# Performance work log

Measured on AMD Instinct MI355X. Metric: run time of the kernel, lower is better.

Reference implementation:

```python
import jax, jax.numpy as jnp
import numpy as np

M1 = M2 = M3 = 8  # truncated Hartley modes (min(modes, in_channels) in original)


def dht(x):
    # Discrete Hartley transform via 3D FFT over spatial axes: real - imag
    r = jnp.fft.fftn(x, axes=(2, 3, 4))
    return r.real - r.imag


def _mul(a, w):
    # 'bixyz,ioxyz->boxyz' mode-wise channel mixing
    return jnp.einsum('bixyz,ioxyz->boxyz', a, w)


def setup_inputs() -> dict:
    key = jax.random.key(0)
    ks = jax.random.split(key, 5)
    B, Ci, Co = 2, 64, 64
    S1 = S2 = S3 = 64
    scale = 1.0 / (Ci * Co)
    x = jax.random.normal(ks[0], (B, Ci, S1, S2, S3), dtype=jnp.float32)
    wshape = (Ci, Co, M1, M2, M3)
    w1 = scale * jax.random.uniform(ks[1], wshape, dtype=jnp.float32)
    w2 = scale * jax.random.uniform(ks[2], wshape, dtype=jnp.float32)
    w3 = scale * jax.random.uniform(ks[3], wshape, dtype=jnp.float32)
    w4 = scale * jax.random.uniform(ks[4], wshape, dtype=jnp.float32)
    return {"x": x, "w1": w1, "w2": w2, "w3": w3, "w4": w4}


def reference(x, w1, w2, w3, w4):
    b, ci, s1, s2, s3 = x.shape
    co = w1.shape[1]
    # Hartley transform of x ("cos part") and of fully flipped x ("sin part")
    xh = dht(x)
    xhf = dht(x[:, :, ::-1, ::-1, ::-1])

    out_ht = jnp.zeros((b, co, s1, s2, s3), dtype=x.dtype)
    out_ht = out_ht.at[:, :, :M1, :M2, :M3].set(_mul(xh[:, :, :M1, :M2, :M3], w1))
    out_ht = out_ht.at[:, :, -M1:, :M2, :M3].set(_mul(xh[:, :, -M1:, :M2, :M3], w2))
    out_ht = out_ht.at[:, :, :M1, -M2:, :M3].set(_mul(xh[:, :, :M1, -M2:, :M3], w3))
    out_ht = out_ht.at[:, :, -M1:, -M2:, :M3].set(_mul(xh[:, :, -M1:, -M2:, :M3], w4))
    # original zeroes out_ht[:, :, M1:, M2:, M3:] — already zero here since 2*modes <= size

    # inverse DHT = DHT / (D*M*N)
    x_rec = dht(out_ht) / (s1 * s2 * s3)

    # phase = angle(complex(cos_part, sin_part)) = atan2(sin, cos), only on corner block; 0 elsewhere
    phase_corner = jnp.arctan2(xhf[:, :, :M1, :M2, :M3], xh[:, :, :M1, :M2, :M3])
    cos_phase = jnp.ones((b, ci, s1, s2, s3), dtype=x.dtype)
    cos_phase = cos_phase.at[:, :, :M1, :M2, :M3].set(jnp.cos(phase_corner))
    return x_rec * cos_phase
```

## Files before the change

kernel.cpp:

```cpp
#include <hip/hip_runtime.h>
#include <math.h>

struct cf2 { float x, y; };
struct TW64 { float c[64], s[64]; };
struct CF2T { cf2 v[64]; };

constexpr double PI_D = 3.14159265358979323846264338327950288;

constexpr double tsin(double x){
  double x2 = x*x, r = x, t = x;
  t *= -x2/6.0;   r += t;
  t *= -x2/20.0;  r += t;
  t *= -x2/42.0;  r += t;
  t *= -x2/72.0;  r += t;
  t *= -x2/110.0; r += t;
  t *= -x2/156.0; r += t;
  t *= -x2/210.0; r += t;
  t *= -x2/272.0; r += t;
  return r;
}
constexpr double tcos(double x){
  double x2 = x*x, r = 1.0, t = 1.0;
  t *= -x2/2.0;   r += t;
  t *= -x2/12.0;  r += t;
  t *= -x2/30.0;  r += t;
  t *= -x2/56.0;  r += t;
  t *= -x2/90.0;  r += t;
  t *= -x2/132.0; r += t;
  t *= -x2/182.0; r += t;
  t *= -x2/240.0; r += t;
  return r;
}
constexpr double ang_cos(int j){
  int r = j & 15, q = (j >> 4) & 3;
  double a = PI_D/32.0 * r;
  double cc = tcos(a), ss = tsin(a);
  return q==0 ? cc : q==1 ? -ss : q==2 ? -cc : ss;
}
constexpr double ang_sin(int j){
  int r = j & 15, q = (j >> 4) & 3;
  double a = PI_D/32.0 * r;
  double cc = tcos(a), ss = tsin(a);
  return q==0 ? ss : q==1 ? cc : q==2 ? -ss : -cc;
}
constexpr TW64 make_tw(){
  TW64 t{};
  for (int j=0;j<64;j++){ t.c[j] = (float)ang_cos(j); t.s[j] = (float)ang_sin(j); }
  return t;
}
constexpr CF2T make_twi(){
  CF2T r{};
  for (int j=0;j<64;j++){ r.v[j].x = (float)ang_cos(j); r.v[j].y = (float)ang_sin(j); }
  return r;
}
constexpr CF2T make_pq(){
  CF2T r{};
  for (int j=0;j<64;j++){
    double c = ang_cos(j), s = ang_sin(j);
    r.v[j].x = (float)((c + s) / 262144.0);
    r.v[j].y = (float)((s - c) / 262144.0);
  }
  return r;
}

constexpr TW64 TWct = make_tw();
__constant__ CF2T TWIdev = make_twi();
__constant__ CF2T PQdev  = make_pq();


template<int G>
__device__ __forceinline__ void stageA4(const float* __restrict__ row, int sw, float* a){
  #pragma unroll
  for (int m=0;m<8;m++) a[m]=0.f;
  #pragma unroll
  for (int qd=0;qd<16;qd++){
    float4 v = ((const float4*)row)[qd ^ sw];
    float xv[4] = {v.x, v.y, v.z, v.w};
    #pragma unroll
    for (int u=0;u<4;u++){
      int n3 = qd*4 + u;
      #pragma unroll
      for (int m=0;m<4;m++){
        a[2*m  ] = fmaf(xv[u],  TWct.c[((G+m)*n3)&63], a[2*m  ]);
        a[2*m+1] = fmaf(xv[u], -TWct.s[((G+m)*n3)&63], a[2*m+1]);
      }
    }
  }
}

__global__ __launch_bounds__(256) void k_fwd(const float* __restrict__ x, float2* __restrict__ y2g){
  __shared__ alignas(16) float xt[2][64][64];
  __shared__ alignas(16) float2 y1[2][8][66];
  __shared__ cf2 twl[64];
  int bid = blockIdx.x;
  int pp = bid & 31, ci_b = bid >> 5;
  int t = threadIdx.x;
  if (t < 64) twl[t] = TWIdev.v[t];

  const float4* src = (const float4*)(x + (size_t)(ci_b*64 + pp*2)*4096);
  #pragma unroll
  for (int j=0;j<8;j++){
    int q = t + j*256;
    float4 v = src[q];
    int n1l = q >> 10, r = q & 1023;
    int n2 = r >> 4, n3q = r & 15;
    float* d = &xt[n1l][n2][(n3q ^ (n2 & 7))*4];
    d[0]=v.x; d[1]=v.y; d[2]=v.z; d[3]=v.w;
  }
  __syncthreads();

  {
    int n2 = t & 63, g = (t>>6)&1, n1l = t>>7;
    const float* row = &xt[n1l][n2][0];
    int sw = n2 & 7;
    float a[8];
    if (g==0) stageA4<0>(row, sw, a); else stageA4<4>(row, sw, a);
    #pragma unroll
    for (int m=0;m<4;m++) y1[n1l][4*g+m][n2] = make_float2(a[2*m], a[2*m+1]);
  }
  __syncthreads();

  {
    int n1l = t>>7, s = t&127, k2i = s>>3, k3 = s&7;
    int k2 = k2i<8 ? k2i : 48+k2i;
    cf2 st = twl[k2];
    float c = 1.f, sn = 0.f, ar = 0.f, ai = 0.f;
    const float4* yrow = (const float4*)&y1[n1l][k3][0];
    #pragma unroll
    for (int m=0;m<32;m++){
      float4 v = yrow[m];
      ar = fmaf(v.x, c, fmaf(v.y, sn, ar));
      ai = fmaf(v.y, c, fmaf(-v.x, sn, ai));
      float c2 = fmaf(c, st.x, -(sn*st.y));
      float s2 = fmaf(sn, st.x,  c*st.y);
      ar = fmaf(v.z, c2, fmaf(v.w, s2, ar));
      ai = fmaf(v.w, c2, fmaf(-v.z, s2, ai));
      c  = fmaf(c2, st.x, -(s2*st.y));
      sn = fmaf(s2, st.x,  c2*st.y);
    }
    y2g[(size_t)(ci_b*64 + pp*2 + n1l)*128 + s] = make_float2(ar, ai);
  }
}

__global__ __launch_bounds__(256) void k_fwd_n1(const float2* __restrict__ y2g,
                                                float* __restrict__ xh, float* __restrict__ cp){
  __shared__ alignas(16) float2 yl[64][8];
  __shared__ cf2 twl[64];
  int bc = blockIdx.x >> 4, k2i = blockIdx.x & 15;
  int t = threadIdx.x;
  if (t < 64) twl[t] = TWIdev.v[t];
  {
    int n1 = t >> 2, q = t & 3;
    const float4* s4 = (const float4*)(y2g + ((size_t)(bc*64 + n1)*128 + k2i*8));
    ((float4*)&yl[n1][0])[q] = s4[q];
  }
  __syncthreads();
  int half = t&1, k3 = (t>>1)&7, k1i = t>>4;
  int k1 = k1i<8 ? k1i : 48+k1i;
  cf2 st = twl[k1];
  cf2 cs = twl[(k1*half*32)&63];
  float c = cs.x, sn = cs.y, ar = 0.f, ai = 0.f;
  #pragma unroll
  for (int i=0;i<32;i++){
    float2 y = yl[half*32+i][k3];
    ar = fmaf(y.x, c, fmaf(y.y, sn, ar));
    ai = fmaf(y.y, c, fmaf(-y.x, sn, ai));
    float c2 = fmaf(c, st.x, -(sn*st.y));
    sn = fmaf(sn, st.x,  c*st.y);
    c = c2;
  }
  ar += __shfl_xor(ar, 1, 64);
  ai += __shfl_xor(ai, 1, 64);
  if (half == 0){
    float vxh = ar - ai;
    xh[(size_t)(bc*16 + k1i)*128 + k2i*8 + k3] = vxh;
    if (k1i < 8 && k2i < 8){
      cf2 tw = twl[(k1i + k2i + k3) & 63];
      float vxhf = ar*(tw.x - tw.y) + ai*(tw.x + tw.y);
      cp[(size_t)bc*512 + k1i*64 + k2i*8 + k3] = cosf(atan2f(vxhf, vxh));
    }
  }
}

__global__ __launch_bounds__(256) void k_mix(const float* __restrict__ xh,
    const float* __restrict__ w1, const float* __restrict__ w2,
    const float* __restrict__ w3, const float* __restrict__ w4,
    float* __restrict__ mh){
  __shared__ alignas(16) float xs[2][64][64];
  __shared__ alignas(16) float wsh[64][64];
  __shared__ float ps[2][128];
  int bid = blockIdx.x;
  int k1l = bid & 7, co = (bid >> 3) & 63, blk = bid >> 9;
  const float* w = (blk==0) ? w1 : (blk==1) ? w2 : (blk==2) ? w3 : w4;
  int k1i = k1l + ((blk & 1) << 3);
  int k2off = (blk & 2) ? 64 : 0;
  int t = threadIdx.x;
  #pragma unroll
  for (int jj=0;jj<4;jj++){
    int idx = t + jj*256;
    int ci = idx >> 4, kq = idx & 15;
    float4 v = *(const float4*)(w + (size_t)(ci*64 + co)*512 + k1l*64 + kq*4);
    ((float4*)&wsh[ci][0])[kq] = v;
  }
  #pragma unroll
  for (int jj=0;jj<8;jj++){
    int idx = t + jj*256;
    int b = idx >> 10, ci = (idx >> 4) & 63, kq = idx & 15;
    float4 v = *(const float4*)(xh + (size_t)((b*64 + ci)*16 + k1i)*128 + k2off + kq*4);
    ((float4*)&xs[b][ci][0])[kq] = v;
  }
  __syncthreads();
  int half = t >> 7, o = t & 127, b = o >> 6, kk = o & 63;
  float acc = 0.f;
  #pragma unroll 8
  for (int i=0;i<32;i++){
    int ci = half*32 + i;
    acc = fmaf(xs[b][ci][kk], wsh[ci][kk], acc);
  }
  ps[half][o] = acc;
  __syncthreads();
  if (t < 128){
    int b2 = t >> 6, kk2 = t & 63;
    mh[(size_t)((b2*64 + co)*16 + k1i)*128 + k2off + kk2] = ps[0][t] + ps[1][t];
  }
}

__global__ __launch_bounds__(256) void k_inv(const float* __restrict__ mh,
                                             const float* __restrict__ cp,
                                             float* __restrict__ out){
  __shared__ alignas(16) float ml[2048];
  __shared__ alignas(16) float2 z1[16][8];
  __shared__ alignas(16) float2 z2[64][8];
  __shared__ cf2 twl[64];
  __shared__ cf2 pql[64];
  int bid = blockIdx.x;
  int n1 = bid & 63, bc = bid >> 6;
  int t = threadIdx.x;
  if (t < 64){ twl[t] = TWIdev.v[t]; pql[t] = PQdev.v[t]; }
  const float4* src = (const float4*)(mh + (size_t)bc * 2048);
  ((float4*)ml)[t]       = src[t];
  ((float4*)ml)[t + 256] = src[t + 256];
  __syncthreads();
  if (t < 128){
    float zr = 0.f, zi = 0.f;
    #pragma unroll
    for (int k1i=0;k1i<16;k1i++){
      int k1 = k1i < 8 ? k1i : 48 + k1i;
      cf2 tw = TWIdev.v[(k1*n1)&63];
      float m = ml[k1i*128 + t];
      zr = fmaf(m, tw.x, zr);
      zi = fmaf(m, -tw.y, zi);
    }
    z1[t>>3][t&7] = make_float2(zr, zi);
  }
  __syncthreads();
  #pragma unroll
  for (int jo=0;jo<2;jo++){
    int o = t + jo*256;
    int n2 = o >> 3, k3 = o & 7;
    cf2 st = twl[n2];
    float zr = 0.f, zi = 0.f;
    float c = 1.f, sn = 0.f;
    #pragma unroll
    for (int k2i=0;k2i<8;k2i++){
      float2 z = z1[k2i][k3];
      zr = fmaf(z.x, c, fmaf(z.y, sn, zr));
      zi = fmaf(z.y, c, fmaf(-z.x, sn, zi));
      float c2 = fmaf(c, st.x, -(sn*st.y));
      sn = fmaf(sn, st.x, c*st.y);
      c = c2;
    }
    cf2 cs = twl[(56*n2)&63];
    c = cs.x; sn = cs.y;
    #pragma unroll
    for (int k2i=8;k2i<16;k2i++){
      float2 z = z1[k2i][k3];
      zr = fmaf(z.x, c, fmaf(z.y, sn, zr));
      zi = fmaf(z.y, c, fmaf(-z.x, sn, zi));
      float c2 = fmaf(c, st.x, -(sn*st.y));
      sn = fmaf(sn, st.x, c*st.y);
      c = c2;
    }
    z2[n2][k3] = make_float2(zr, zi);
  }
  __syncthreads();
  int n3p = t & 31;
  int wv = t >> 6, g = (t >> 5) & 1;
  int n30 = 2*n3p, n31 = 2*n3p + 1;
  float p0[8], q0[8], p1[8], q1[8];
  #pragma unroll
  for (int k3=0;k3<8;k3++){
    cf2 a = pql[(k3*n30)&63];
    cf2 b = pql[(k3*n31)&63];
    p0[k3] = a.x; q0[k3] = a.y;
    p1[k3] = b.x; q1[k3] = b.y;
  }
  float* orow = out + ((size_t)bc*64 + n1)*4096;
  const float* cprow = cp + (size_t)bc*512 + n1*64;
  bool corner = (n1 < 8) && (n3p < 4);
  #pragma unroll
  for (int j=0;j<8;j++){
    int n2 = wv*16 + 2*j + g;
    const float4* zr4 = (const float4*)&z2[n2][0];
    float4 u0 = zr4[0], u1 = zr4[1], u2 = zr4[2], u3 = zr4[3];
    float v0, v1;
    v0 = fmaf(u0.x, p0[0], u0.y*q0[0]);
    v0 = fmaf(u0.z, p0[1], fmaf(u0.w, q0[1], v0));
    v0 = fmaf(u1.x, p0[2], fmaf(u1.y, q0[2], v0));
    v0 = fmaf(u1.z, p0[3], fmaf(u1.w, q0[3], v0));
    v0 = fmaf(u2.x, p0[4], fmaf(u2.y, q0[4], v0));
    v0 = fmaf(u2.z, p0[5], fmaf(u2.w, q0[5], v0));
    v0 = fmaf(u3.x, p0[6], fmaf(u3.y, q0[6], v0));
    v0 = fmaf(u3.z, p0[7], fmaf(u3.w, q0[7], v0));
    v1 = fmaf(u0.x, p1[0], u0.y*q1[0]);
    v1 = fmaf(u0.z, p1[1], fmaf(u0.w, q1[1], v1));
    v1 = fmaf(u1.x, p1[2], fmaf(u1.y, q1[2], v1));
    v1 = fmaf(u1.z, p1[3], fmaf(u1.w, q1[3], v1));
    v1 = fmaf(u2.x, p1[4], fmaf(u2.y, q1[4], v1));
    v1 = fmaf(u2.z, p1[5], fmaf(u2.w, q1[5], v1));
    v1 = fmaf(u3.x, p1[6], fmaf(u3.y, q1[6], v1));
    v1 = fmaf(u3.z, p1[7], fmaf(u3.w, q1[7], v1));
    if (corner && n2 < 8){
      v0 *= cprow[n2*8 + n30];
      v1 *= cprow[n2*8 + n31];
    }
    ((float2*)orow)[n2*32 + n3p] = make_float2(v0, v1);
  }
}

extern "C" void kernel_launch(void* const* d_in, const int* in_sizes, int n_in,
                              void* d_out, int out_size, void* d_ws, size_t ws_size,
                              hipStream_t stream) {
  (void)in_sizes; (void)n_in; (void)out_size; (void)ws_size;
  const float* x  = (const float*)d_in[0];
  const float* w1 = (const float*)d_in[1];
  const float* w2 = (const float*)d_in[2];
  const float* w3 = (const float*)d_in[3];
  const float* w4 = (const float*)d_in[4];
  float* out = (float*)d_out;
  char* ws = (char*)d_ws;
  float2* y2g = (float2*)ws;
  float*  xh  = (float*)(ws + (8u<<20));
  float*  cp  = (float*)(ws + (9u<<20));
  float*  mh  = (float*)(ws + (9u<<20) + (256u<<10));

  k_fwd   <<<4096, 256, 0, stream>>>(x, y2g);
  k_fwd_n1<<<2048, 256, 0, stream>>>(y2g, xh, cp);
  k_mix   <<<2048, 256, 0, stream>>>(xh, w1, w2, w3, w4, mh);
  k_inv   <<<8192, 256, 0, stream>>>(mh, cp, out);
}
```

Before: 283.9 us.

## Fuse four kernels into one persistent kernel with grid-wide barriers

Replaces the four separate launches (forward 2D DFT, forward n1 DFT, channel mix, inverse transform) with a single persistent kernel of 512 blocks that loops over tiles and separates the phases with atomic-counter grid barriers. Stage buffers are unioned in shared memory, and the first stage prefetches the next input tile into shared memory while the previous one is processed. This removes launch overheads and inter-kernel gaps, but parallelism drops to 512 blocks and the spin barriers depend on every block being co-resident. The input stage now runs one 64x64 slice per iteration with fewer threads active in the second DFT step.

```diff
diff --git a/kernel.cpp b/kernel.cpp
--- a/kernel.cpp
+++ b/kernel.cpp
@@ -67,11 +67,30 @@
 __constant__ CF2T TWIdev = make_twi();
 __constant__ CF2T PQdev  = make_pq();
 
-
-template<int G>
-__device__ __forceinline__ void stageA4(const float* __restrict__ row, int sw, float* a){
-  #pragma unroll
-  for (int m=0;m<8;m++) a[m]=0.f;
+#define NB 512
+
+__device__ __forceinline__ void gridbar(unsigned* bar){
+  __syncthreads();
+  __threadfence();
+  if (threadIdx.x == 0){
+    atomicAdd(bar, 1u);
+    while (__hip_atomic_load(bar, __ATOMIC_ACQUIRE, __HIP_MEMORY_SCOPE_AGENT) < (unsigned)NB)
+      __builtin_amdgcn_s_sleep(2);
+  }
+  __syncthreads();
+  __threadfence();
+}
+
+union SMem {
+  struct { float xt[64][64]; float2 y1[8][66]; } s1;
+  struct { float2 yl[64][8]; } s2;
+  struct { float wsh[64][64]; float xs[64][64]; float ps[4][64]; } s3;
+  struct { float ml[2048]; float2 z1[16][8]; float2 z2[64][8]; } s4;
+};
+
+template<int K>
+__device__ __forceinline__ void stageA2(const float* __restrict__ row, int sw, float* a){
+  a[0]=a[1]=a[2]=a[3]=0.f;
   #pragma unroll
   for (int qd=0;qd<16;qd++){
     float4 v = ((const float4*)row)[qd ^ sw];
@@ -79,252 +98,270 @@
     #pragma unroll
     for (int u=0;u<4;u++){
       int n3 = qd*4 + u;
-      #pragma unroll
-      for (int m=0;m<4;m++){
-        a[2*m  ] = fmaf(xv[u],  TWct.c[((G+m)*n3)&63], a[2*m  ]);
-        a[2*m+1] = fmaf(xv[u], -TWct.s[((G+m)*n3)&63], a[2*m+1]);
-      }
-    }
-  }
-}
-
-__global__ __launch_bounds__(256) void k_fwd(const float* __restrict__ x, float2* __restrict__ y2g){
-  __shared__ alignas(16) float xt[2][64][64];
-  __shared__ alignas(16) float2 y1[2][8][66];
-  __shared__ cf2 twl[64];
-  int bid = blockIdx.x;
-  int pp = bid & 31, ci_b = bid >> 5;
-  int t = threadIdx.x;
-  if (t < 64) twl[t] = TWIdev.v[t];
-
-  const float4* src = (const float4*)(x + (size_t)(ci_b*64 + pp*2)*4096);
+      a[0] = fmaf(xv[u],  TWct.c[((K  )*n3)&63], a[0]);
+      a[1] = fmaf(xv[u], -TWct.s[((K  )*n3)&63], a[1]);
+      a[2] = fmaf(xv[u],  TWct.c[((K+1)*n3)&63], a[2]);
+      a[3] = fmaf(xv[u], -TWct.s[((K+1)*n3)&63], a[3]);
+    }
+  }
+}
+
+__device__ __forceinline__ void s1_load(const float* __restrict__ x, SMem& sm, int tile, int t){
+  const float4* src = (const float4*)(x + (size_t)tile*4096);
   #pragma unroll
-  for (int j=0;j<8;j++){
+  for (int j=0;j<4;j++){
     int q = t + j*256;
     float4 v = src[q];
-    int n1l = q >> 10, r = q & 1023;
-    int n2 = r >> 4, n3q = r & 15;
-    float* d = &xt[n1l][n2][(n3q ^ (n2 & 7))*4];
+    int n2 = q >> 4, n3q = q & 15;
+    float* d = &sm.s1.xt[n2][(n3q ^ (n2 & 7))*4];
     d[0]=v.x; d[1]=v.y; d[2]=v.z; d[3]=v.w;
   }
-  __syncthreads();
-
-  {
-    int n2 = t & 63, g = (t>>6)&1, n1l = t>>7;
-    const float* row = &xt[n1l][n2][0];
-    int sw = n2 & 7;
-    float a[8];
-    if (g==0) stageA4<0>(row, sw, a); else stageA4<4>(row, sw, a);
-    #pragma unroll
-    for (int m=0;m<4;m++) y1[n1l][4*g+m][n2] = make_float2(a[2*m], a[2*m+1]);
-  }
-  __syncthreads();
-
-  {
-    int n1l = t>>7, s = t&127, k2i = s>>3, k3 = s&7;
-    int k2 = k2i<8 ? k2i : 48+k2i;
-    cf2 st = twl[k2];
-    float c = 1.f, sn = 0.f, ar = 0.f, ai = 0.f;
-    const float4* yrow = (const float4*)&y1[n1l][k3][0];
-    #pragma unroll
-    for (int m=0;m<32;m++){
-      float4 v = yrow[m];
-      ar = fmaf(v.x, c, fmaf(v.y, sn, ar));
-      ai = fmaf(v.y, c, fmaf(-v.x, sn, ai));
-      float c2 = fmaf(c, st.x, -(sn*st.y));
-      float s2 = fmaf(sn, st.x,  c*st.y);
-      ar = fmaf(v.z, c2, fmaf(v.w, s2, ar));
-      ai = fmaf(v.w, c2, fmaf(-v.z, s2, ai));
-      c  = fmaf(c2, st.x, -(s2*st.y));
-      sn = fmaf(s2, st.x,  c2*st.y);
-    }
-    y2g[(size_t)(ci_b*64 + pp*2 + n1l)*128 + s] = make_float2(ar, ai);
-  }
-}
-
-__global__ __launch_bounds__(256) void k_fwd_n1(const float2* __restrict__ y2g,
-                                                float* __restrict__ xh, float* __restrict__ cp){
-  __shared__ alignas(16) float2 yl[64][8];
-  __shared__ cf2 twl[64];
-  int bc = blockIdx.x >> 4, k2i = blockIdx.x & 15;
-  int t = threadIdx.x;
-  if (t < 64) twl[t] = TWIdev.v[t];
-  {
-    int n1 = t >> 2, q = t & 3;
-    const float4* s4 = (const float4*)(y2g + ((size_t)(bc*64 + n1)*128 + k2i*8));
-    ((float4*)&yl[n1][0])[q] = s4[q];
-  }
-  __syncthreads();
-  int half = t&1, k3 = (t>>1)&7, k1i = t>>4;
-  int k1 = k1i<8 ? k1i : 48+k1i;
-  cf2 st = twl[k1];
-  cf2 cs = twl[(k1*half*32)&63];
-  float c = cs.x, sn = cs.y, ar = 0.f, ai = 0.f;
-  #pragma unroll
-  for (int i=0;i<32;i++){
-    float2 y = yl[half*32+i][k3];
-    ar = fmaf(y.x, c, fmaf(y.y, sn, ar));
-    ai = fmaf(y.y, c, fmaf(-y.x, sn, ai));
-    float c2 = fmaf(c, st.x, -(sn*st.y));
-    sn = fmaf(sn, st.x,  c*st.y);
-    c = c2;
-  }
-  ar += __shfl_xor(ar, 1, 64);
-  ai += __shfl_xor(ai, 1, 64);
-  if (half == 0){
-    float vxh = ar - ai;
-    xh[(size_t)(bc*16 + k1i)*128 + k2i*8 + k3] = vxh;
-    if (k1i < 8 && k2i < 8){
-      cf2 tw = twl[(k1i + k2i + k3) & 63];
-      float vxhf = ar*(tw.x - tw.y) + ai*(tw.x + tw.y);
-      cp[(size_t)bc*512 + k1i*64 + k2i*8 + k3] = cosf(atan2f(vxhf, vxh));
-    }
-  }
-}
-
-__global__ __launch_bounds__(256) void k_mix(const float* __restrict__ xh,
+}
+
+__global__ __launch_bounds__(256, 2) void k_all(
+    const float* __restrict__ x,
     const float* __restrict__ w1, const float* __restrict__ w2,
     const float* __restrict__ w3, const float* __restrict__ w4,
-    float* __restrict__ mh){
-  __shared__ alignas(16) float xs[2][64][64];
-  __shared__ alignas(16) float wsh[64][64];
-  __shared__ float ps[2][128];
-  int bid = blockIdx.x;
-  int k1l = bid & 7, co = (bid >> 3) & 63, blk = bid >> 9;
-  const float* w = (blk==0) ? w1 : (blk==1) ? w2 : (blk==2) ? w3 : w4;
-  int k1i = k1l + ((blk & 1) << 3);
-  int k2off = (blk & 2) ? 64 : 0;
-  int t = threadIdx.x;
-  #pragma unroll
-  for (int jj=0;jj<4;jj++){
-    int idx = t + jj*256;
-    int ci = idx >> 4, kq = idx & 15;
-    float4 v = *(const float4*)(w + (size_t)(ci*64 + co)*512 + k1l*64 + kq*4);
-    ((float4*)&wsh[ci][0])[kq] = v;
-  }
-  #pragma unroll
-  for (int jj=0;jj<8;jj++){
-    int idx = t + jj*256;
-    int b = idx >> 10, ci = (idx >> 4) & 63, kq = idx & 15;
-    float4 v = *(const float4*)(xh + (size_t)((b*64 + ci)*16 + k1i)*128 + k2off + kq*4);
-    ((float4*)&xs[b][ci][0])[kq] = v;
-  }
-  __syncthreads();
-  int half = t >> 7, o = t & 127, b = o >> 6, kk = o & 63;
-  float acc = 0.f;
-  #pragma unroll 8
-  for (int i=0;i<32;i++){
-    int ci = half*32 + i;
-    acc = fmaf(xs[b][ci][kk], wsh[ci][kk], acc);
-  }
-  ps[half][o] = acc;
-  __syncthreads();
-  if (t < 128){
-    int b2 = t >> 6, kk2 = t & 63;
-    mh[(size_t)((b2*64 + co)*16 + k1i)*128 + k2off + kk2] = ps[0][t] + ps[1][t];
-  }
-}
-
-__global__ __launch_bounds__(256) void k_inv(const float* __restrict__ mh,
-                                             const float* __restrict__ cp,
-                                             float* __restrict__ out){
-  __shared__ alignas(16) float ml[2048];
-  __shared__ alignas(16) float2 z1[16][8];
-  __shared__ alignas(16) float2 z2[64][8];
+    float2* __restrict__ y2g, float* __restrict__ xh, float* __restrict__ cp,
+    float* __restrict__ mh, float* __restrict__ out, unsigned* __restrict__ bars)
+{
+  __shared__ SMem sm;
   __shared__ cf2 twl[64];
   __shared__ cf2 pql[64];
+  int t = threadIdx.x;
   int bid = blockIdx.x;
-  int n1 = bid & 63, bc = bid >> 6;
-  int t = threadIdx.x;
   if (t < 64){ twl[t] = TWIdev.v[t]; pql[t] = PQdev.v[t]; }
-  const float4* src = (const float4*)(mh + (size_t)bc * 2048);
-  ((float4*)ml)[t]       = src[t];
-  ((float4*)ml)[t + 256] = src[t + 256];
-  __syncthreads();
-  if (t < 128){
-    float zr = 0.f, zi = 0.f;
+
+  {
+    int tile0 = bid * 16;
+    s1_load(x, sm, tile0, t);
+    __syncthreads();
+    #pragma unroll 1
+    for (int i=0;i<16;i++){
+      int tile = tile0 + i;
+      {
+        int n2 = t & 63, g = t >> 6;
+        const float* row = &sm.s1.xt[n2][0];
+        int sw = n2 & 7;
+        float a[4];
+        switch(g){
+          case 0: stageA2<0>(row, sw, a); break;
+          case 1: stageA2<2>(row, sw, a); break;
+          case 2: stageA2<4>(row, sw, a); break;
+          default: stageA2<6>(row, sw, a); break;
+        }
+        sm.s1.y1[2*g  ][n2] = make_float2(a[0], a[1]);
+        sm.s1.y1[2*g+1][n2] = make_float2(a[2], a[3]);
+      }
+      __syncthreads();
+      if (i < 15) s1_load(x, sm, tile+1, t);
+      if (t < 128){
+        int k2i = t>>3, k3 = t&7;
+        int k2 = k2i<8 ? k2i : 48+k2i;
+        cf2 st = twl[k2];
+        float c = 1.f, sn = 0.f, ar = 0.f, ai = 0.f;
+        const float4* yrow = (const float4*)&sm.s1.y1[k3][0];
+        #pragma unroll
+        for (int m=0;m<32;m++){
+          float4 v = yrow[m];
+          ar = fmaf(v.x, c, fmaf(v.y, sn, ar));
+          ai = fmaf(v.y, c, fmaf(-v.x, sn, ai));
+          float c2 = fmaf(c, st.x, -(sn*st.y));
+          float s2 = fmaf(sn, st.x,  c*st.y);
+          ar = fmaf(v.z, c2, fmaf(v.w, s2, ar));
+          ai = fmaf(v.w, c2, fmaf(-v.z, s2, ai));
+          c  = fmaf(c2, st.x, -(s2*st.y));
+          sn = fmaf(s2, st.x,  c2*st.y);
+        }
+        y2g[(size_t)tile*128 + t] = make_float2(ar, ai);
+      }
+      __syncthreads();
+    }
+  }
+  gridbar(bars + 0);
+
+  #pragma unroll 1
+  for (int i=0;i<4;i++){
+    int tile = bid*4 + i;
+    int bc = tile >> 4, k2i = tile & 15;
+    {
+      int n1 = t >> 2, q = t & 3;
+      const float4* s4p = (const float4*)(y2g + ((size_t)(bc*64 + n1)*128 + k2i*8));
+      ((float4*)&sm.s2.yl[n1][0])[q] = s4p[q];
+    }
+    __syncthreads();
+    {
+      int half = t&1, k3 = (t>>1)&7, k1i = t>>4;
+      int k1 = k1i<8 ? k1i : 48+k1i;
+      cf2 st = twl[k1];
+      cf2 cs = twl[(k1*half*32)&63];
+      float c = cs.x, sn = cs.y, ar = 0.f, ai = 0.f;
+      #pragma unroll
+      for (int j=0;j<32;j++){
+        float2 y = sm.s2.yl[half*32+j][k3];
+        ar = fmaf(y.x, c, fmaf(y.y, sn, ar));
+        ai = fmaf(y.y, c, fmaf(-y.x, sn, ai));
+        float c2 = fmaf(c, st.x, -(sn*st.y));
+        sn = fmaf(sn, st.x,  c*st.y);
+        c = c2;
+      }
+      ar += __shfl_xor(ar, 1, 64);
+      ai += __shfl_xor(ai, 1, 64);
+      if (half == 0){
+        float vxh = ar - ai;
+        xh[(size_t)(bc*16 + k1i)*128 + k2i*8 + k3] = vxh;
+        if (k1i < 8 && k2i < 8){
+          cf2 tw = twl[(k1i + k2i + k3) & 63];
+          float vxhf = ar*(tw.x - tw.y) + ai*(tw.x + tw.y);
+          cp[(size_t)bc*512 + k1i*64 + k2i*8 + k3] = cosf(atan2f(vxhf, vxh));
+        }
+      }
+    }
+    __syncthreads();
+  }
+  gridbar(bars + 1);
+
+  #pragma unroll 1
+  for (int i=0;i<4;i++){
+    int tile = bid*4 + i;
+    int k1l = tile & 7, co = (tile >> 3) & 63, blk = tile >> 9;
+    const float* w = (blk==0) ? w1 : (blk==1) ? w2 : (blk==2) ? w3 : w4;
+    int k1i = k1l + ((blk & 1) << 3);
+    int k2off = (blk & 2) ? 64 : 0;
     #pragma unroll
-    for (int k1i=0;k1i<16;k1i++){
-      int k1 = k1i < 8 ? k1i : 48 + k1i;
-      cf2 tw = TWIdev.v[(k1*n1)&63];
-      float m = ml[k1i*128 + t];
-      zr = fmaf(m, tw.x, zr);
-      zi = fmaf(m, -tw.y, zi);
-    }
-    z1[t>>3][t&7] = make_float2(zr, zi);
-  }
-  __syncthreads();
-  #pragma unroll
-  for (int jo=0;jo<2;jo++){
-    int o = t + jo*256;
-    int n2 = o >> 3, k3 = o & 7;
-    cf2 st = twl[n2];
-    float zr = 0.f, zi = 0.f;
-    float c = 1.f, sn = 0.f;
-    #pragma unroll
-    for (int k2i=0;k2i<8;k2i++){
-      float2 z = z1[k2i][k3];
-      zr = fmaf(z.x, c, fmaf(z.y, sn, zr));
-      zi = fmaf(z.y, c, fmaf(-z.x, sn, zi));
-      float c2 = fmaf(c, st.x, -(sn*st.y));
-      sn = fmaf(sn, st.x, c*st.y);
-      c = c2;
-    }
-    cf2 cs = twl[(56*n2)&63];
-    c = cs.x; sn = cs.y;
-    #pragma unroll
-    for (int k2i=8;k2i<16;k2i++){
-      float2 z = z1[k2i][k3];
-      zr = fmaf(z.x, c, fmaf(z.y, sn, zr));
-      zi = fmaf(z.y, c, fmaf(-z.x, sn, zi));
-      float c2 = fmaf(c, st.x, -(sn*st.y));
-      sn = fmaf(sn, st.x, c*st.y);
-      c = c2;
-    }
-    z2[n2][k3] = make_float2(zr, zi);
-  }
-  __syncthreads();
-  int n3p = t & 31;
-  int wv = t >> 6, g = (t >> 5) & 1;
-  int n30 = 2*n3p, n31 = 2*n3p + 1;
-  float p0[8], q0[8], p1[8], q1[8];
-  #pragma unroll
-  for (int k3=0;k3<8;k3++){
-    cf2 a = pql[(k3*n30)&63];
-    cf2 b = pql[(k3*n31)&63];
-    p0[k3] = a.x; q0[k3] = a.y;
-    p1[k3] = b.x; q1[k3] = b.y;
-  }
-  float* orow = out + ((size_t)bc*64 + n1)*4096;
-  const float* cprow = cp + (size_t)bc*512 + n1*64;
-  bool corner = (n1 < 8) && (n3p < 4);
-  #pragma unroll
-  for (int j=0;j<8;j++){
-    int n2 = wv*16 + 2*j + g;
-    const float4* zr4 = (const float4*)&z2[n2][0];
-    float4 u0 = zr4[0], u1 = zr4[1], u2 = zr4[2], u3 = zr4[3];
-    float v0, v1;
-    v0 = fmaf(u0.x, p0[0], u0.y*q0[0]);
-    v0 = fmaf(u0.z, p0[1], fmaf(u0.w, q0[1], v0));
-    v0 = fmaf(u1.x, p0[2], fmaf(u1.y, q0[2], v0));
-    v0 = fmaf(u1.z, p0[3], fmaf(u1.w, q0[3], v0));
-    v0 = fmaf(u2.x, p0[4], fmaf(u2.y, q0[4], v0));
-    v0 = fmaf(u2.z, p0[5], fmaf(u2.w, q0[5], v0));
-    v0 = fmaf(u3.x, p0[6], fmaf(u3.y, q0[6], v0));
-    v0 = fmaf(u3.z, p0[7], fmaf(u3.w, q0[7], v0));
-    v1 = fmaf(u0.x, p1[0], u0.y*q1[0]);
-    v1 = fmaf(u0.z, p1[1], fmaf(u0.w, q1[1], v1));
-    v1 = fmaf(u1.x, p1[2], fmaf(u1.y, q1[2], v1));
-    v1 = fmaf(u1.z, p1[3], fmaf(u1.w, q1[3], v1));
-    v1 = fmaf(u2.x, p1[4], fmaf(u2.y, q1[4], v1));
-    v1 = fmaf(u2.z, p1[5], fmaf(u2.w, q1[5], v1));
-    v1 = fmaf(u3.x, p1[6], fmaf(u3.y, q1[6], v1));
-    v1 = fmaf(u3.z, p1[7], fmaf(u3.w, q1[7], v1));
-    if (corner && n2 < 8){
-      v0 *= cprow[n2*8 + n30];
-      v1 *= cprow[n2*8 + n31];
-    }
-    ((float2*)orow)[n2*32 + n3p] = make_float2(v0, v1);
+    for (int jj=0;jj<4;jj++){
+      int idx = t + jj*256;
+      int ci = idx >> 4, kq = idx & 15;
+      float4 v = *(const float4*)(w + (size_t)(ci*64 + co)*512 + k1l*64 + kq*4);
+      ((float4*)&sm.s3.wsh[ci][0])[kq] = v;
+    }
+    #pragma unroll 1
+    for (int b=0;b<2;b++){
+      #pragma unroll
+      for (int jj=0;jj<4;jj++){
+        int idx = t + jj*256;
+        int ci = idx >> 4, kq = idx & 15;
+        float4 v = *(const float4*)(xh + (size_t)((b*64 + ci)*16 + k1i)*128 + k2off + kq*4);
+        ((float4*)&sm.s3.xs[ci][0])[kq] = v;
+      }
+      __syncthreads();
+      {
+        int quarter = t >> 6, kk = t & 63;
+        float acc = 0.f;
+        #pragma unroll
+        for (int c2=0;c2<16;c2++){
+          int ci = quarter*16 + c2;
+          acc = fmaf(sm.s3.xs[ci][kk], sm.s3.wsh[ci][kk], acc);
+        }
+        sm.s3.ps[quarter][kk] = acc;
+      }
+      __syncthreads();
+      if (t < 64)
+        mh[(size_t)((b*64 + co)*16 + k1i)*128 + k2off + t] =
+          sm.s3.ps[0][t] + sm.s3.ps[1][t] + sm.s3.ps[2][t] + sm.s3.ps[3][t];
+      __syncthreads();
+    }
+  }
+  gridbar(bars + 2);
+
+  {
+    int bc = bid >> 2;
+    const float4* srcm = (const float4*)(mh + (size_t)bc * 2048);
+    ((float4*)sm.s4.ml)[t]       = srcm[t];
+    ((float4*)sm.s4.ml)[t + 256] = srcm[t + 256];
+    __syncthreads();
+    #pragma unroll 1
+    for (int i=0;i<16;i++){
+      int n1 = (bid & 3)*16 + i;
+      if (t < 128){
+        float zr = 0.f, zi = 0.f;
+        #pragma unroll
+        for (int k1i=0;k1i<16;k1i++){
+          int k1 = k1i < 8 ? k1i : 48 + k1i;
+          cf2 tw = TWIdev.v[(k1*n1)&63];
+          float m = sm.s4.ml[k1i*128 + t];
+          zr = fmaf(m, tw.x, zr);
+          zi = fmaf(m, -tw.y, zi);
+        }
+        sm.s4.z1[t>>3][t&7] = make_float2(zr, zi);
+      }
+      __syncthreads();
+      #pragma unroll
+      for (int jo=0;jo<2;jo++){
+        int o = t + jo*256;
+        int n2 = o >> 3, k3 = o & 7;
+        cf2 st = twl[n2];
+        float zr = 0.f, zi = 0.f;
+        float c = 1.f, sn = 0.f;
+        #pragma unroll
+        for (int k2i=0;k2i<8;k2i++){
+          float2 z = sm.s4.z1[k2i][k3];
+          zr = fmaf(z.x, c, fmaf(z.y, sn, zr));
+          zi = fmaf(z.y, c, fmaf(-z.x, sn, zi));
+          float c2 = fmaf(c, st.x, -(sn*st.y));
+          sn = fmaf(sn, st.x, c*st.y);
+          c = c2;
+        }
+        cf2 cs = twl[(56*n2)&63];
+        c = cs.x; sn = cs.y;
+        #pragma unroll
+        for (int k2i=8;k2i<16;k2i++){
+          float2 z = sm.s4.z1[k2i][k3];
+          zr = fmaf(z.x, c, fmaf(z.y, sn, zr));
+          zi = fmaf(z.y, c, fmaf(-z.x, sn, zi));
+          float c2 = fmaf(c, st.x, -(sn*st.y));
+          sn = fmaf(sn, st.x, c*st.y);
+          c = c2;
+        }
+        sm.s4.z2[n2][k3] = make_float2(zr, zi);
+      }
+      __syncthreads();
+      {
+        int n3p = t & 31;
+        int wv = t >> 6, g = (t >> 5) & 1;
+        int n30 = 2*n3p, n31 = 2*n3p + 1;
+        float p0[8], q0[8], p1[8], q1[8];
+        #pragma unroll
+        for (int k3=0;k3<8;k3++){
+          cf2 a = pql[(k3*n30)&63];
+          cf2 b = pql[(k3*n31)&63];
+          p0[k3] = a.x; q0[k3] = a.y;
+          p1[k3] = b.x; q1[k3] = b.y;
+        }
+        float* orow = out + ((size_t)bc*64 + n1)*4096;
+        const float* cprow = cp + (size_t)bc*512 + n1*64;
+        bool corner = (n1 < 8) && (n3p < 4);
+        #pragma unroll
+        for (int j=0;j<8;j++){
+          int n2 = wv*16 + 2*j + g;
+          const float4* zr4 = (const float4*)&sm.s4.z2[n2][0];
+          float4 u0 = zr4[0], u1 = zr4[1], u2 = zr4[2], u3 = zr4[3];
+          float v0, v1;
+          v0 = fmaf(u0.x, p0[0], u0.y*q0[0]);
+          v0 = fmaf(u0.z, p0[1], fmaf(u0.w, q0[1], v0));
+          v0 = fmaf(u1.x, p0[2], fmaf(u1.y, q0[2], v0));
+          v0 = fmaf(u1.z, p0[3], fmaf(u1.w, q0[3], v0));
+          v0 = fmaf(u2.x, p0[4], fmaf(u2.y, q0[4], v0));
+          v0 = fmaf(u2.z, p0[5], fmaf(u2.w, q0[5], v0));
+          v0 = fmaf(u3.x, p0[6], fmaf(u3.y, q0[6], v0));
+          v0 = fmaf(u3.z, p0[7], fmaf(u3.w, q0[7], v0));
+          v1 = fmaf(u0.x, p1[0], u0.y*q1[0]);
+          v1 = fmaf(u0.z, p1[1], fmaf(u0.w, q1[1], v1));
+          v1 = fmaf(u1.x, p1[2], fmaf(u1.y, q1[2], v1));
+          v1 = fmaf(u1.z, p1[3], fmaf(u1.w, q1[3], v1));
+          v1 = fmaf(u2.x, p1[4], fmaf(u2.y, q1[4], v1));
+          v1 = fmaf(u2.z, p1[5], fmaf(u2.w, q1[5], v1));
+          v1 = fmaf(u3.x, p1[6], fmaf(u3.y, q1[6], v1));
+          v1 = fmaf(u3.z, p1[7], fmaf(u3.w, q1[7], v1));
+          if (corner && n2 < 8){
+            v0 *= cprow[n2*8 + n30];
+            v1 *= cprow[n2*8 + n31];
+          }
+          ((float2*)orow)[n2*32 + n3p] = make_float2(v0, v1);
+        }
+      }
+      __syncthreads();
+    }
   }
 }
 
@@ -339,13 +376,13 @@
   const float* w4 = (const float*)d_in[4];
   float* out = (float*)d_out;
   char* ws = (char*)d_ws;
-  float2* y2g = (float2*)ws;
-  float*  xh  = (float*)(ws + (8u<<20));
-  float*  cp  = (float*)(ws + (9u<<20));
-  float*  mh  = (float*)(ws + (9u<<20) + (256u<<10));
-
-  k_fwd   <<<4096, 256, 0, stream>>>(x, y2g);
-  k_fwd_n1<<<2048, 256, 0, stream>>>(y2g, xh, cp);
-  k_mix   <<<2048, 256, 0, stream>>>(xh, w1, w2, w3, w4, mh);
-  k_inv   <<<8192, 256, 0, stream>>>(mh, cp, out);
-}
+  float2*   y2g  = (float2*)ws;
+  float*    xh   = (float*)(ws + (8u<<20));
+  float*    cp   = (float*)(ws + (9u<<20));
+  float*    mh   = (float*)(ws + (9u<<20) + (256u<<10));
+  unsigned* bars = (unsigned*)(ws + (10u<<20) + (512u<<10));
+
+  hipMemsetAsync(bars, 0, 3*sizeof(unsigned), stream);
+
+  k_all<<<NB, 256, 0, stream>>>(x, w1, w2, w3, w4, y2g, xh, cp, mh, out, bars);
+}
```

Result: slower. 631.4 us (+122.4%).

## Split forward DFT stages across more threads and break twiddle recurrence chains

Applied to the files above, without the earlier changes.

k_fwd now handles one (b,ci,n1) plane per block instead of two, launching twice as many blocks. Each thread computes two k3 outputs in stage A instead of four. The k2 stage is split across two half-block groups, combined through shared memory. k_fwd_n1 and k_inv split their serial twiddle-rotation recurrences into two independent chains to expose ILP, and k_mix reads xh directly from global memory across four ci-quarters instead of staging it in shared memory. The aim is more parallelism and shorter dependency chains in these small-DFT stages, at the cost of extra reductions, extra syncs, and less contiguous global reads in k_mix.

```diff
diff --git a/kernel.cpp b/kernel.cpp
--- a/kernel.cpp
+++ b/kernel.cpp
@@ -68,10 +68,9 @@
 __constant__ CF2T PQdev  = make_pq();
 
 
-template<int G>
-__device__ __forceinline__ void stageA4(const float* __restrict__ row, int sw, float* a){
-  #pragma unroll
-  for (int m=0;m<8;m++) a[m]=0.f;
+template<int K>
+__device__ __forceinline__ void stageA2(const float* __restrict__ row, int sw, float* a){
+  a[0]=a[1]=a[2]=a[3]=0.f;
   #pragma unroll
   for (int qd=0;qd<16;qd++){
     float4 v = ((const float4*)row)[qd ^ sw];
@@ -79,66 +78,88 @@
     #pragma unroll
     for (int u=0;u<4;u++){
       int n3 = qd*4 + u;
-      #pragma unroll
-      for (int m=0;m<4;m++){
-        a[2*m  ] = fmaf(xv[u],  TWct.c[((G+m)*n3)&63], a[2*m  ]);
-        a[2*m+1] = fmaf(xv[u], -TWct.s[((G+m)*n3)&63], a[2*m+1]);
-      }
+      a[0] = fmaf(xv[u],  TWct.c[((K  )*n3)&63], a[0]);
+      a[1] = fmaf(xv[u], -TWct.s[((K  )*n3)&63], a[1]);
+      a[2] = fmaf(xv[u],  TWct.c[((K+1)*n3)&63], a[2]);
+      a[3] = fmaf(xv[u], -TWct.s[((K+1)*n3)&63], a[3]);
     }
   }
 }
 
 __global__ __launch_bounds__(256) void k_fwd(const float* __restrict__ x, float2* __restrict__ y2g){
-  __shared__ alignas(16) float xt[2][64][64];
-  __shared__ alignas(16) float2 y1[2][8][66];
+  __shared__ alignas(16) float xt[64][64];
+  __shared__ alignas(16) float2 y1[8][66];
+  __shared__ float2 ps[2][128];
   __shared__ cf2 twl[64];
   int bid = blockIdx.x;
-  int pp = bid & 31, ci_b = bid >> 5;
   int t = threadIdx.x;
   if (t < 64) twl[t] = TWIdev.v[t];
 
-  const float4* src = (const float4*)(x + (size_t)(ci_b*64 + pp*2)*4096);
-  #pragma unroll
-  for (int j=0;j<8;j++){
+  const float4* src = (const float4*)(x + (size_t)bid*4096);
+  #pragma unroll
+  for (int j=0;j<4;j++){
     int q = t + j*256;
     float4 v = src[q];
-    int n1l = q >> 10, r = q & 1023;
-    int n2 = r >> 4, n3q = r & 15;
-    float* d = &xt[n1l][n2][(n3q ^ (n2 & 7))*4];
+    int n2 = q >> 4, n3q = q & 15;
+    float* d = &xt[n2][(n3q ^ (n2 & 7))*4];
     d[0]=v.x; d[1]=v.y; d[2]=v.z; d[3]=v.w;
   }
   __syncthreads();
 
   {
-    int n2 = t & 63, g = (t>>6)&1, n1l = t>>7;
-    const float* row = &xt[n1l][n2][0];
+    int n2 = t & 63, g = t >> 6;
+    const float* row = &xt[n2][0];
     int sw = n2 & 7;
-    float a[8];
-    if (g==0) stageA4<0>(row, sw, a); else stageA4<4>(row, sw, a);
-    #pragma unroll
-    for (int m=0;m<4;m++) y1[n1l][4*g+m][n2] = make_float2(a[2*m], a[2*m+1]);
+    float a[4];
+    switch(g){
+      case 0: stageA2<0>(row, sw, a); break;
+      case 1: stageA2<2>(row, sw, a); break;
+      case 2: stageA2<4>(row, sw, a); break;
+      default: stageA2<6>(row, sw, a); break;
+    }
+    y1[2*g  ][n2] = make_float2(a[0], a[1]);
+    y1[2*g+1][n2] = make_float2(a[2], a[3]);
   }
   __syncthreads();
 
   {
-    int n1l = t>>7, s = t&127, k2i = s>>3, k3 = s&7;
+    int s = t & 127, h = t >> 7;
+    int k2i = s>>3, k3 = s&7;
     int k2 = k2i<8 ? k2i : 48+k2i;
     cf2 st = twl[k2];
-    float c = 1.f, sn = 0.f, ar = 0.f, ai = 0.f;
-    const float4* yrow = (const float4*)&y1[n1l][k3][0];
-    #pragma unroll
-    for (int m=0;m<32;m++){
-      float4 v = yrow[m];
-      ar = fmaf(v.x, c, fmaf(v.y, sn, ar));
-      ai = fmaf(v.y, c, fmaf(-v.x, sn, ai));
-      float c2 = fmaf(c, st.x, -(sn*st.y));
-      float s2 = fmaf(sn, st.x,  c*st.y);
-      ar = fmaf(v.z, c2, fmaf(v.w, s2, ar));
-      ai = fmaf(v.w, c2, fmaf(-v.z, s2, ai));
-      c  = fmaf(c2, st.x, -(s2*st.y));
-      sn = fmaf(s2, st.x,  c2*st.y);
-    }
-    y2g[(size_t)(ci_b*64 + pp*2 + n1l)*128 + s] = make_float2(ar, ai);
+    cf2 i0 = twl[(k2*32*h) & 63];
+    cf2 i1 = twl[(k2*(32*h+16)) & 63];
+    float c0=i0.x, s0=i0.y, ar0=0.f, ai0=0.f;
+    float c1=i1.x, s1=i1.y, ar1=0.f, ai1=0.f;
+    const float4* yrow = (const float4*)&y1[k3][0];
+    #pragma unroll
+    for (int m=0;m<8;m++){
+      float4 v = yrow[16*h + m];
+      ar0 = fmaf(v.x, c0, fmaf(v.y, s0, ar0));
+      ai0 = fmaf(v.y, c0, fmaf(-v.x, s0, ai0));
+      float c0b = fmaf(c0, st.x, -(s0*st.y));
+      float s0b = fmaf(s0, st.x,  c0*st.y);
+      ar0 = fmaf(v.z, c0b, fmaf(v.w, s0b, ar0));
+      ai0 = fmaf(v.w, c0b, fmaf(-v.z, s0b, ai0));
+      c0  = fmaf(c0b, st.x, -(s0b*st.y));
+      s0  = fmaf(s0b, st.x,  c0b*st.y);
+
+      float4 w = yrow[16*h + 8 + m];
+      ar1 = fmaf(w.x, c1, fmaf(w.y, s1, ar1));
+      ai1 = fmaf(w.y, c1, fmaf(-w.x, s1, ai1));
+      float c1b = fmaf(c1, st.x, -(s1*st.y));
+      float s1b = fmaf(s1, st.x,  c1*st.y);
+      ar1 = fmaf(w.z, c1b, fmaf(w.w, s1b, ar1));
+      ai1 = fmaf(w.w, c1b, fmaf(-w.z, s1b, ai1));
+      c1  = fmaf(c1b, st.x, -(s1b*st.y));
+      s1  = fmaf(s1b, st.x,  c1b*st.y);
+    }
+    ps[h][s] = make_float2(ar0+ar1, ai0+ai1);
+  }
+  __syncthreads();
+  if (t < 128){
+    float2 a = ps[0][t], b = ps[1][t];
+    y2g[(size_t)bid*128 + t] = make_float2(a.x+b.x, a.y+b.y);
   }
 }
 
@@ -158,17 +179,26 @@
   int half = t&1, k3 = (t>>1)&7, k1i = t>>4;
   int k1 = k1i<8 ? k1i : 48+k1i;
   cf2 st = twl[k1];
-  cf2 cs = twl[(k1*half*32)&63];
-  float c = cs.x, sn = cs.y, ar = 0.f, ai = 0.f;
-  #pragma unroll
-  for (int i=0;i<32;i++){
-    float2 y = yl[half*32+i][k3];
-    ar = fmaf(y.x, c, fmaf(y.y, sn, ar));
-    ai = fmaf(y.y, c, fmaf(-y.x, sn, ai));
-    float c2 = fmaf(c, st.x, -(sn*st.y));
-    sn = fmaf(sn, st.x,  c*st.y);
-    c = c2;
-  }
+  cf2 i0 = twl[(k1*32*half)&63];
+  cf2 i1 = twl[(k1*(32*half+16))&63];
+  float c0=i0.x, s0=i0.y, ar0=0.f, ai0=0.f;
+  float c1=i1.x, s1=i1.y, ar1=0.f, ai1=0.f;
+  #pragma unroll
+  for (int j=0;j<16;j++){
+    float2 y = yl[half*32+j][k3];
+    ar0 = fmaf(y.x, c0, fmaf(y.y, s0, ar0));
+    ai0 = fmaf(y.y, c0, fmaf(-y.x, s0, ai0));
+    float c0b = fmaf(c0, st.x, -(s0*st.y));
+    s0 = fmaf(s0, st.x,  c0*st.y);
+    c0 = c0b;
+    float2 z = yl[half*32+16+j][k3];
+    ar1 = fmaf(z.x, c1, fmaf(z.y, s1, ar1));
+    ai1 = fmaf(z.y, c1, fmaf(-z.x, s1, ai1));
+    float c1b = fmaf(c1, st.x, -(s1*st.y));
+    s1 = fmaf(s1, st.x,  c1*st.y);
+    c1 = c1b;
+  }
+  float ar = ar0 + ar1, ai = ai0 + ai1;
   ar += __shfl_xor(ar, 1, 64);
   ai += __shfl_xor(ai, 1, 64);
   if (half == 0){
@@ -186,9 +216,8 @@
     const float* __restrict__ w1, const float* __restrict__ w2,
     const float* __restrict__ w3, const float* __restrict__ w4,
     float* __restrict__ mh){
-  __shared__ alignas(16) float xs[2][64][64];
   __shared__ alignas(16) float wsh[64][64];
-  __shared__ float ps[2][128];
+  __shared__ float ps[4][64];
   int bid = blockIdx.x;
   int k1l = bid & 7, co = (bid >> 3) & 63, blk = bid >> 9;
   const float* w = (blk==0) ? w1 : (blk==1) ? w2 : (blk==2) ? w3 : w4;
@@ -202,26 +231,22 @@
     float4 v = *(const float4*)(w + (size_t)(ci*64 + co)*512 + k1l*64 + kq*4);
     ((float4*)&wsh[ci][0])[kq] = v;
   }
-  #pragma unroll
-  for (int jj=0;jj<8;jj++){
-    int idx = t + jj*256;
-    int b = idx >> 10, ci = (idx >> 4) & 63, kq = idx & 15;
-    float4 v = *(const float4*)(xh + (size_t)((b*64 + ci)*16 + k1i)*128 + k2off + kq*4);
-    ((float4*)&xs[b][ci][0])[kq] = v;
-  }
-  __syncthreads();
-  int half = t >> 7, o = t & 127, b = o >> 6, kk = o & 63;
-  float acc = 0.f;
-  #pragma unroll 8
-  for (int i=0;i<32;i++){
-    int ci = half*32 + i;
-    acc = fmaf(xs[b][ci][kk], wsh[ci][kk], acc);
-  }
-  ps[half][o] = acc;
-  __syncthreads();
-  if (t < 128){
-    int b2 = t >> 6, kk2 = t & 63;
-    mh[(size_t)((b2*64 + co)*16 + k1i)*128 + k2off + kk2] = ps[0][t] + ps[1][t];
+  __syncthreads();
+  int quarter = t >> 6, kk = t & 63;
+  #pragma unroll 1
+  for (int b=0;b<2;b++){
+    const float* xb = xh + ((size_t)(b*64 + quarter*16)*16 + k1i)*128 + k2off + kk;
+    float acc = 0.f;
+    #pragma unroll
+    for (int c2=0;c2<16;c2++){
+      acc = fmaf(xb[(size_t)c2*2048], wsh[quarter*16 + c2][kk], acc);
+    }
+    ps[quarter][kk] = acc;
+    __syncthreads();
+    if (t < 64)
+      mh[(size_t)((b*64 + co)*16 + k1i)*128 + k2off + t] =
+        ps[0][t] + ps[1][t] + ps[2][t] + ps[3][t];
+    __syncthreads();
   }
 }
 
@@ -259,72 +284,71 @@
     int o = t + jo*256;
     int n2 = o >> 3, k3 = o & 7;
     cf2 st = twl[n2];
-    float zr = 0.f, zi = 0.f;
-    float c = 1.f, sn = 0.f;
-    #pragma unroll
-    for (int k2i=0;k2i<8;k2i++){
-      float2 z = z1[k2i][k3];
-      zr = fmaf(z.x, c, fmaf(z.y, sn, zr));
-      zi = fmaf(z.y, c, fmaf(-z.x, sn, zi));
-      float c2 = fmaf(c, st.x, -(sn*st.y));
-      sn = fmaf(sn, st.x, c*st.y);
-      c = c2;
-    }
-    cf2 cs = twl[(56*n2)&63];
-    c = cs.x; sn = cs.y;
-    #pragma unroll
-    for (int k2i=8;k2i<16;k2i++){
-      float2 z = z1[k2i][k3];
-      zr = fmaf(z.x, c, fmaf(z.y, sn, zr));
-      zi = fmaf(z.y, c, fmaf(-z.x, sn, zi));
-      float c2 = fmaf(c, st.x, -(sn*st.y));
-      sn = fmaf(sn, st.x, c*st.y);
-      c = c2;
-    }
-    z2[n2][k3] = make_float2(zr, zi);
-  }
-  __syncthreads();
-  int n3p = t & 31;
-  int wv = t >> 6, g = (t >> 5) & 1;
-  int n30 = 2*n3p, n31 = 2*n3p + 1;
-  float p0[8], q0[8], p1[8], q1[8];
-  #pragma unroll
-  for (int k3=0;k3<8;k3++){
-    cf2 a = pql[(k3*n30)&63];
-    cf2 b = pql[(k3*n31)&63];
-    p0[k3] = a.x; q0[k3] = a.y;
-    p1[k3] = b.x; q1[k3] = b.y;
-  }
-  float* orow = out + ((size_t)bc*64 + n1)*4096;
-  const float* cprow = cp + (size_t)bc*512 + n1*64;
-  bool corner = (n1 < 8) && (n3p < 4);
-  #pragma unroll
-  for (int j=0;j<8;j++){
-    int n2 = wv*16 + 2*j + g;
-    const float4* zr4 = (const float4*)&z2[n2][0];
-    float4 u0 = zr4[0], u1 = zr4[1], u2 = zr4[2], u3 = zr4[3];
-    float v0, v1;
-    v0 = fmaf(u0.x, p0[0], u0.y*q0[0]);
-    v0 = fmaf(u0.z, p0[1], fmaf(u0.w, q0[1], v0));
-    v0 = fmaf(u1.x, p0[2], fmaf(u1.y, q0[2], v0));
-    v0 = fmaf(u1.z, p0[3], fmaf(u1.w, q0[3], v0));
-    v0 = fmaf(u2.x, p0[4], fmaf(u2.y, q0[4], v0));
-    v0 = fmaf(u2.z, p0[5], fmaf(u2.w, q0[5], v0));
-    v0 = fmaf(u3.x, p0[6], fmaf(u3.y, q0[6], v0));
-    v0 = fmaf(u3.z, p0[7], fmaf(u3.w, q0[7], v0));
-    v1 = fmaf(u0.x, p1[0], u0.y*q1[0]);
-    v1 = fmaf(u0.z, p1[1], fmaf(u0.w, q1[1], v1));
-    v1 = fmaf(u1.x, p1[2], fmaf(u1.y, q1[2], v1));
-    v1 = fmaf(u1.z, p1[3], fmaf(u1.w, q1[3], v1));
-    v1 = fmaf(u2.x, p1[4], fmaf(u2.y, q1[4], v1));
-    v1 = fmaf(u2.z, p1[5], fmaf(u2.w, q1[5], v1));
-    v1 = fmaf(u3.x, p1[6], fmaf(u3.y, q1[6], v1));
-    v1 = fmaf(u3.z, p1[7], fmaf(u3.w, q1[7], v1));
-    if (corner && n2 < 8){
-      v0 *= cprow[n2*8 + n30];
-      v1 *= cprow[n2*8 + n31];
-    }
-    ((float2*)orow)[n2*32 + n3p] = make_float2(v0, v1);
+    float zr0=0.f, zi0=0.f, zr1=0.f, zi1=0.f;
+    float c0 = 1.f, s0 = 0.f;
+    cf2 i1 = twl[(56*n2)&63];
+    float c1 = i1.x, s1 = i1.y;
+    #pragma unroll
+    for (int k=0;k<8;k++){
+      float2 a = z1[k][k3];
+      zr0 = fmaf(a.x, c0, fmaf(a.y, s0, zr0));
+      zi0 = fmaf(a.y, c0, fmaf(-a.x, s0, zi0));
+      float c0b = fmaf(c0, st.x, -(s0*st.y));
+      s0 = fmaf(s0, st.x, c0*st.y);
+      c0 = c0b;
+      float2 b = z1[8+k][k3];
+      zr1 = fmaf(b.x, c1, fmaf(b.y, s1, zr1));
+      zi1 = fmaf(b.y, c1, fmaf(-b.x, s1, zi1));
+      float c1b = fmaf(c1, st.x, -(s1*st.y));
+      s1 = fmaf(s1, st.x, c1*st.y);
+      c1 = c1b;
+    }
+    z2[n2][k3] = make_float2(zr0+zr1, zi0+zi1);
+  }
+  __syncthreads();
+  {
+    int n3p = t & 31;
+    int wv = t >> 6, g = (t >> 5) & 1;
+    int n30 = 2*n3p, n31 = 2*n3p + 1;
+    float p0[8], q0[8], p1[8], q1[8];
+    #pragma unroll
+    for (int k3=0;k3<8;k3++){
+      cf2 a = pql[(k3*n30)&63];
+      cf2 b = pql[(k3*n31)&63];
+      p0[k3] = a.x; q0[k3] = a.y;
+      p1[k3] = b.x; q1[k3] = b.y;
+    }
+    float* orow = out + ((size_t)bc*64 + n1)*4096;
+    const float* cprow = cp + (size_t)bc*512 + n1*64;
+    bool corner = (n1 < 8) && (n3p < 4);
+    #pragma unroll
+    for (int j=0;j<8;j++){
+      int n2 = wv*16 + 2*j + g;
+      const float4* zr4 = (const float4*)&z2[n2][0];
+      float4 u0 = zr4[0], u1 = zr4[1], u2 = zr4[2], u3 = zr4[3];
+      float v0, v1;
+      v0 = fmaf(u0.x, p0[0], u0.y*q0[0]);
+      v0 = fmaf(u0.z, p0[1], fmaf(u0.w, q0[1], v0));
+      v0 = fmaf(u1.x, p0[2], fmaf(u1.y, q0[2], v0));
+      v0 = fmaf(u1.z, p0[3], fmaf(u1.w, q0[3], v0));
+      v0 = fmaf(u2.x, p0[4], fmaf(u2.y, q0[4], v0));
+      v0 = fmaf(u2.z, p0[5], fmaf(u2.w, q0[5], v0));
+      v0 = fmaf(u3.x, p0[6], fmaf(u3.y, q0[6], v0));
+      v0 = fmaf(u3.z, p0[7], fmaf(u3.w, q0[7], v0));
+      v1 = fmaf(u0.x, p1[0], u0.y*q1[0]);
+      v1 = fmaf(u0.z, p1[1], fmaf(u0.w, q1[1], v1));
+      v1 = fmaf(u1.x, p1[2], fmaf(u1.y, q1[2], v1));
+      v1 = fmaf(u1.z, p1[3], fmaf(u1.w, q1[3], v1));
+      v1 = fmaf(u2.x, p1[4], fmaf(u2.y, q1[4], v1));
+      v1 = fmaf(u2.z, p1[5], fmaf(u2.w, q1[5], v1));
+      v1 = fmaf(u3.x, p1[6], fmaf(u3.y, q1[6], v1));
+      v1 = fmaf(u3.z, p1[7], fmaf(u3.w, q1[7], v1));
+      if (corner && n2 < 8){
+        v0 *= cprow[n2*8 + n30];
+        v1 *= cprow[n2*8 + n31];
+      }
+      ((float2*)orow)[n2*32 + n3p] = make_float2(v0, v1);
+    }
   }
 }
 
@@ -344,7 +368,7 @@
   float*  cp  = (float*)(ws + (9u<<20));
   float*  mh  = (float*)(ws + (9u<<20) + (256u<<10));
 
-  k_fwd   <<<4096, 256, 0, stream>>>(x, y2g);
+  k_fwd   <<<8192, 256, 0, stream>>>(x, y2g);
   k_fwd_n1<<<2048, 256, 0, stream>>>(y2g, xh, cp);
   k_mix   <<<2048, 256, 0, stream>>>(xh, w1, w2, w3, w4, mh);
   k_inv   <<<8192, 256, 0, stream>>>(mh, cp, out);
```

Measured after the change: 288.0 us. Within noise of the previous version (+1.5%).
